# Kernel optimization log

Measured on AMD Instinct MI355X. Metric: run time of the kernel, lower is better.

Reference implementation:

```python
import jax, jax.numpy as jnp
import numpy as np

HIDDEN = 100  # hard-coded in the torch module


def setup_inputs() -> dict:
    key = jax.random.key(0)
    k1, k2, k3, k4, k5 = jax.random.split(key, 5)
    dims, N, M = 32, 4096, 8192
    centroids = jax.random.normal(k1, (N, dims), dtype=jnp.float32)
    x = jax.random.normal(k2, (M, dims), dtype=jnp.float32)
    # torch Linear params: y = x @ W.T (+ b)
    W1 = jax.random.normal(k3, (HIDDEN, dims), dtype=jnp.float32) / np.sqrt(dims)
    W2 = jax.random.normal(k4, (dims, HIDDEN), dtype=jnp.float32) / np.sqrt(HIDDEN)
    b2 = jax.random.uniform(k5, (dims,), dtype=jnp.float32, minval=-0.1, maxval=0.1)
    return {"centroids": centroids, "x": x, "W1": W1, "W2": W2, "b2": b2}


def reference(centroids, x, W1, W2, b2):
    dims = centroids.shape[1]
    # small MLP: Linear(dims,100,no bias) -> Linear(100,dims) -> tanh, then gate by centroids
    loc = jnp.tanh((centroids @ W1.T) @ W2.T + b2) * centroids  # [N, dims]
    # covariance = eye(dims) * var(centroids) (scalar, unbiased var over all elements)
    var = jnp.var(centroids, ddof=1)
    # diagonal-Gaussian log_prob, pairwise [N, M] via ||x-loc||^2 expansion (no NxMxD cube)
    sq = (
        jnp.sum(x * x, axis=1)[None, :]
        + jnp.sum(loc * loc, axis=1)[:, None]
        - 2.0 * (loc @ x.T)
    )  # [N, M]
    log_norm = dims * jnp.log(2.0 * jnp.pi * var)
    logp = -0.5 * (sq / var + log_norm)  # [N, M]
    return jnp.exp(logp).T  # [M, N]
```

## Files before the change

### kernel.cpp

```cpp
#include <hip/hip_runtime.h>
#include <math.h>

#define DIMS 32
#define NROWS 4096
#define MROWS 8192
#define HID 100

#define L2E 1.44269504088896340736f

typedef float f32x4 __attribute__((ext_vector_type(4)));
typedef short bf16x8 __attribute__((ext_vector_type(8)));

__device__ __forceinline__ void load_var(const float* part, float& iv, float& var) {
    float S = 0.0f, Q = 0.0f;
    #pragma unroll
    for (int i = 0; i < 8; i++) { S += part[2 * i]; Q += part[2 * i + 1]; }
    const float cnt = (float)(NROWS * DIMS);
    var = (Q - S * S / cnt) / (cnt - 1.0f);
    iv = 1.0f / var;
}

__device__ __forceinline__ float tanh_fast(float x) {
    float xc = fminf(fmaxf(x, -10.0f), 10.0f);
    float e = __builtin_amdgcn_exp2f(xc * (2.0f * L2E));
    return (e - 1.0f) * __builtin_amdgcn_rcpf(e + 1.0f);
}

__device__ __forceinline__ unsigned short f2bf(float f) {
    unsigned int u = __float_as_uint(f);
    u += 0x7FFFu + ((u >> 16) & 1u);
    return (unsigned short)(u >> 16);
}

__global__ __launch_bounds__(256) void k_prep(const float* __restrict__ cent,
                                              const float* __restrict__ x,
                                              const float* __restrict__ W1,
                                              const float* __restrict__ W2,
                                              const float* __restrict__ b2,
                                              float* __restrict__ part,
                                              float* __restrict__ A,
                                              float* __restrict__ B,
                                              unsigned short* __restrict__ xb,
                                              unsigned short* __restrict__ locb) {
    int b = blockIdx.x, t = threadIdx.x;

    if (b < 8) {
        const float4* c4 = (const float4*)cent;
        float s = 0.0f, q = 0.0f;
        #pragma unroll
        for (int i = 0; i < 16; i++) {
            float4 a = c4[b * 4096 + i * 256 + t];
            s += a.x + a.y + a.z + a.w;
            q += a.x * a.x + a.y * a.y + a.z * a.z + a.w * a.w;
        }
        #pragma unroll
        for (int off = 32; off > 0; off >>= 1) {
            s += __shfl_down(s, off);
            q += __shfl_down(q, off);
        }
        __shared__ float red[8];
        int lane = t & 63, wid = t >> 6;
        if (lane == 0) { red[wid] = s; red[4 + wid] = q; }
        __syncthreads();
        if (t == 0) {
            part[2 * b]     = red[0] + red[1] + red[2] + red[3];
            part[2 * b + 1] = red[4] + red[5] + red[6] + red[7];
        }
    } else if (b < 24) {
        __shared__ float w1s[HID * DIMS];
        __shared__ float w2s[DIMS * HID];
        __shared__ __align__(16) float ms[DIMS * DIMS];
        __shared__ float b2s[DIMS];
        for (int i = t; i < HID * DIMS; i += 256) { w1s[i] = W1[i]; w2s[i] = W2[i]; }
        if (t < DIMS) b2s[t] = b2[t];
        __syncthreads();
        #pragma unroll
        for (int o = 0; o < 4; o++) {
            int id = o * 256 + t;
            int r = id >> 5, cc = id & 31;
            float a = 0.0f;
            for (int j = 0; j < HID; j++) a += w2s[r * HID + j] * w1s[j * DIMS + cc];
            ms[id] = a;
        }
        __syncthreads();

        int n = (b - 8) * 256 + t;
        float c[DIMS];
        const float4* cr = (const float4*)(cent + (size_t)n * DIMS);
        #pragma unroll
        for (int i = 0; i < 8; i++) {
            float4 v = cr[i];
            c[4 * i] = v.x; c[4 * i + 1] = v.y; c[4 * i + 2] = v.z; c[4 * i + 3] = v.w;
        }
        float lr[DIMS];
        float lsq = 0.0f;
        #pragma unroll
        for (int d = 0; d < DIMS; d++) {
            const float4* mr = (const float4*)&ms[d * DIMS];
            float a0 = 0.f, a1 = 0.f, a2 = 0.f, a3 = 0.f;
            #pragma unroll
            for (int kk = 0; kk < 8; kk++) {
                float4 m = mr[kk];
                a0 += c[4 * kk] * m.x;
                a1 += c[4 * kk + 1] * m.y;
                a2 += c[4 * kk + 2] * m.z;
                a3 += c[4 * kk + 3] * m.w;
            }
            float v = tanh_fast((a0 + a1) + (a2 + a3) + b2s[d]) * c[d];
            lr[d] = v;
            lsq += v * v;
        }
        unsigned int w[16];
        #pragma unroll
        for (int d = 0; d < 16; d++)
            w[d] = (unsigned int)f2bf(lr[2 * d]) | ((unsigned int)f2bf(lr[2 * d + 1]) << 16);
        uint4* lo = (uint4*)(locb + (size_t)n * DIMS);
        lo[0] = make_uint4(w[0], w[1], w[2], w[3]);
        lo[1] = make_uint4(w[4], w[5], w[6], w[7]);
        lo[2] = make_uint4(w[8], w[9], w[10], w[11]);
        lo[3] = make_uint4(w[12], w[13], w[14], w[15]);
        B[n] = lsq;
    } else {
        int m = (b - 24) * 256 + t;
        const float4* xr = (const float4*)(x + (size_t)m * DIMS);
        float xsq = 0.0f;
        unsigned int w[16];
        #pragma unroll
        for (int i = 0; i < 8; i++) {
            float4 v = xr[i];
            xsq += v.x * v.x + v.y * v.y + v.z * v.z + v.w * v.w;
            w[2 * i]     = (unsigned int)f2bf(v.x) | ((unsigned int)f2bf(v.y) << 16);
            w[2 * i + 1] = (unsigned int)f2bf(v.z) | ((unsigned int)f2bf(v.w) << 16);
        }
        uint4* xo = (uint4*)(xb + (size_t)m * DIMS);
        xo[0] = make_uint4(w[0], w[1], w[2], w[3]);
        xo[1] = make_uint4(w[4], w[5], w[6], w[7]);
        xo[2] = make_uint4(w[8], w[9], w[10], w[11]);
        xo[3] = make_uint4(w[12], w[13], w[14], w[15]);
        A[m] = xsq;
    }
}

__global__ __launch_bounds__(256) void k_pair(const unsigned short* __restrict__ xb,
                                              const unsigned short* __restrict__ locb,
                                              const float* __restrict__ A,
                                              const float* __restrict__ B,
                                              const float* __restrict__ part,
                                              float* __restrict__ out) {
    float iv, var;
    load_var(part, iv, var);
    const float s  = L2E * iv;
    const float hv = -0.5f * L2E * iv;
    const float C0 = -16.0f * log2f(2.0f * (float)M_PI * var);

    int t = threadIdx.x;
    int lane = t & 63, wid = t >> 6;
    int bid = blockIdx.x;
    int tile = ((bid & 7) << 8) | (bid >> 3);
    int mt = tile >> 5, ntl = tile & 31;
    int m0 = mt * 128 + (wid >> 1) * 64;
    int n0 = ntl * 128 + (wid & 1) * 64;
    int r = lane & 15, g = lane >> 4;

    bf16x8 lf[4], xf[4];
    #pragma unroll
    for (int j = 0; j < 4; j++)
        lf[j] = *(const bf16x8*)(locb + (size_t)(n0 + 16 * j + r) * DIMS + 8 * g);
    #pragma unroll
    for (int i = 0; i < 4; i++)
        xf[i] = *(const bf16x8*)(xb + (size_t)(m0 + 16 * i + r) * DIMS + 8 * g);

    f32x4 zero = {0.0f, 0.0f, 0.0f, 0.0f};
    f32x4 acc[4][4];
    #pragma unroll
    for (int j = 0; j < 4; j++)
        #pragma unroll
        for (int i = 0; i < 4; i++)
            acc[j][i] = __builtin_amdgcn_mfma_f32_16x16x32_bf16(lf[j], xf[i], zero, 0, 0, 0);

    float em[4];
    #pragma unroll
    for (int i = 0; i < 4; i++)
        em[i] = fmaf(hv, A[m0 + 16 * i + r], C0);
    f32x4 en[4];
    #pragma unroll
    for (int j = 0; j < 4; j++) {
        float4 bv = *(const float4*)&B[n0 + 16 * j + 4 * g];
        en[j].x = hv * bv.x; en[j].y = hv * bv.y; en[j].z = hv * bv.z; en[j].w = hv * bv.w;
    }

    #pragma unroll
    for (int i = 0; i < 4; i++) {
        float* orow = out + (size_t)(m0 + 16 * i + r) * NROWS;
        float e = em[i];
        #pragma unroll
        for (int j = 0; j < 4; j++) {
            f32x4 v;
            v.x = __builtin_amdgcn_exp2f(fmaf(s, acc[j][i][0], e + en[j].x));
            v.y = __builtin_amdgcn_exp2f(fmaf(s, acc[j][i][1], e + en[j].y));
            v.z = __builtin_amdgcn_exp2f(fmaf(s, acc[j][i][2], e + en[j].z));
            v.w = __builtin_amdgcn_exp2f(fmaf(s, acc[j][i][3], e + en[j].w));
            *(f32x4*)(orow + n0 + 16 * j + 4 * g) = v;
        }
    }
}

extern "C" void kernel_launch(void* const* d_in, const int* in_sizes, int n_in,
                              void* d_out, int out_size, void* d_ws, size_t ws_size,
                              hipStream_t stream) {
    const float* cent = (const float*)d_in[0];
    const float* x    = (const float*)d_in[1];
    const float* W1   = (const float*)d_in[2];
    const float* W2   = (const float*)d_in[3];
    const float* b2   = (const float*)d_in[4];
    float* out = (float*)d_out;

    float* ws   = (float*)d_ws;
    float* part = ws;
    float* A    = ws + 64;
    float* B    = A + MROWS;
    unsigned short* xb   = (unsigned short*)(B + NROWS);
    unsigned short* locb = xb + (size_t)MROWS * DIMS;

    k_prep<<<56, 256, 0, stream>>>(cent, x, W1, W2, b2, part, A, B, xb, locb);
    k_pair<<<NROWS / 128 * (MROWS / 128), 256, 0, stream>>>(xb, locb, A, B, part, out);
}
```

Measured before the change: 159.5 us.

## Fuse loc MLP and bf16 packing into pairwise kernel via shared memory

The prep kernel no longer writes bf16 loc/x and the squared norms to global memory. It now only computes the variance partials and the 32x32 combined weight matrix. Each pairwise tile block recomputes the MLP for its 128 centroids and packs its 128 x rows to bf16 in padded LDS, then runs the MFMA and exp epilogue. This removes the large prep kernel and a global round trip, at the cost of redundant MLP and conversion work in every one of the 2048 tile blocks. The prep critical path also shrinks to 8 blocks, with block 0 handling the weight product.

```diff
diff --git a/kernel.cpp b/kernel.cpp
--- a/kernel.cpp
+++ b/kernel.cpp
@@ -8,6 +8,8 @@
 
 #define L2E 1.44269504088896340736f
 
+#define LROW 40
+
 typedef float f32x4 __attribute__((ext_vector_type(4)));
 typedef short bf16x8 __attribute__((ext_vector_type(8)));
 
@@ -32,47 +34,37 @@
     return (unsigned short)(u >> 16);
 }
 
-__global__ __launch_bounds__(256) void k_prep(const float* __restrict__ cent,
-                                              const float* __restrict__ x,
-                                              const float* __restrict__ W1,
-                                              const float* __restrict__ W2,
-                                              const float* __restrict__ b2,
-                                              float* __restrict__ part,
-                                              float* __restrict__ A,
-                                              float* __restrict__ B,
-                                              unsigned short* __restrict__ xb,
-                                              unsigned short* __restrict__ locb) {
+__global__ __launch_bounds__(256) void k_var(const float* __restrict__ c,
+                                             const float* __restrict__ W1,
+                                             const float* __restrict__ W2,
+                                             float* __restrict__ part,
+                                             float* __restrict__ Mmat) {
     int b = blockIdx.x, t = threadIdx.x;
-
-    if (b < 8) {
-        const float4* c4 = (const float4*)cent;
-        float s = 0.0f, q = 0.0f;
-        #pragma unroll
-        for (int i = 0; i < 16; i++) {
-            float4 a = c4[b * 4096 + i * 256 + t];
-            s += a.x + a.y + a.z + a.w;
-            q += a.x * a.x + a.y * a.y + a.z * a.z + a.w * a.w;
-        }
-        #pragma unroll
-        for (int off = 32; off > 0; off >>= 1) {
-            s += __shfl_down(s, off);
-            q += __shfl_down(q, off);
-        }
-        __shared__ float red[8];
-        int lane = t & 63, wid = t >> 6;
-        if (lane == 0) { red[wid] = s; red[4 + wid] = q; }
-        __syncthreads();
-        if (t == 0) {
-            part[2 * b]     = red[0] + red[1] + red[2] + red[3];
-            part[2 * b + 1] = red[4] + red[5] + red[6] + red[7];
-        }
-    } else if (b < 24) {
+    const float4* c4 = (const float4*)c;
+    float s = 0.0f, q = 0.0f;
+    #pragma unroll
+    for (int i = 0; i < 16; i++) {
+        float4 a = c4[b * 4096 + i * 256 + t];
+        s += a.x + a.y + a.z + a.w;
+        q += a.x * a.x + a.y * a.y + a.z * a.z + a.w * a.w;
+    }
+    #pragma unroll
+    for (int off = 32; off > 0; off >>= 1) {
+        s += __shfl_down(s, off);
+        q += __shfl_down(q, off);
+    }
+    __shared__ float red[8];
+    int lane = t & 63, wid = t >> 6;
+    if (lane == 0) { red[wid] = s; red[4 + wid] = q; }
+    __syncthreads();
+    if (t == 0) {
+        part[2 * b]     = red[0] + red[1] + red[2] + red[3];
+        part[2 * b + 1] = red[4] + red[5] + red[6] + red[7];
+    }
+    if (b == 0) {
         __shared__ float w1s[HID * DIMS];
         __shared__ float w2s[DIMS * HID];
-        __shared__ __align__(16) float ms[DIMS * DIMS];
-        __shared__ float b2s[DIMS];
         for (int i = t; i < HID * DIMS; i += 256) { w1s[i] = W1[i]; w2s[i] = W2[i]; }
-        if (t < DIMS) b2s[t] = b2[t];
         __syncthreads();
         #pragma unroll
         for (int o = 0; o < 4; o++) {
@@ -80,13 +72,46 @@
             int r = id >> 5, cc = id & 31;
             float a = 0.0f;
             for (int j = 0; j < HID; j++) a += w2s[r * HID + j] * w1s[j * DIMS + cc];
-            ms[id] = a;
-        }
-        __syncthreads();
-
-        int n = (b - 8) * 256 + t;
+            Mmat[id] = a;
+        }
+    }
+}
+
+__global__ __launch_bounds__(256) void k_fused(const float* __restrict__ cent,
+                                               const float* __restrict__ x,
+                                               const float* __restrict__ b2,
+                                               const float* __restrict__ part,
+                                               const float* __restrict__ Mmat,
+                                               float* __restrict__ out) {
+    __shared__ __align__(16) float ms[DIMS * DIMS];
+    __shared__ float b2s[DIMS];
+    __shared__ __align__(16) unsigned short ls[128 * LROW];
+    __shared__ __align__(16) unsigned short xs[128 * LROW];
+    __shared__ float As[128];
+    __shared__ float Bs[128];
+
+    float iv, var;
+    load_var(part, iv, var);
+    const float s  = L2E * iv;
+    const float hv = -0.5f * L2E * iv;
+    const float C0 = -16.0f * log2f(2.0f * (float)M_PI * var);
+
+    int t = threadIdx.x;
+    int lane = t & 63, wid = t >> 6;
+    int bid = blockIdx.x;
+    int tile = ((bid & 7) << 8) | (bid >> 3);
+    int mt = tile >> 5, ntl = tile & 31;
+    int mb = mt * 128, nb = ntl * 128;
+
+    #pragma unroll
+    for (int i = 0; i < 4; i++) ms[i * 256 + t] = Mmat[i * 256 + t];
+    if (t < DIMS) b2s[t] = b2[t];
+    __syncthreads();
+
+    if (t < 128) {
+        int row = t;
         float c[DIMS];
-        const float4* cr = (const float4*)(cent + (size_t)n * DIMS);
+        const float4* cr = (const float4*)(cent + (size_t)(nb + row) * DIMS);
         #pragma unroll
         for (int i = 0; i < 8; i++) {
             float4 v = cr[i];
@@ -110,65 +135,53 @@
             lr[d] = v;
             lsq += v * v;
         }
-        unsigned int w[16];
-        #pragma unroll
-        for (int d = 0; d < 16; d++)
-            w[d] = (unsigned int)f2bf(lr[2 * d]) | ((unsigned int)f2bf(lr[2 * d + 1]) << 16);
-        uint4* lo = (uint4*)(locb + (size_t)n * DIMS);
-        lo[0] = make_uint4(w[0], w[1], w[2], w[3]);
-        lo[1] = make_uint4(w[4], w[5], w[6], w[7]);
-        lo[2] = make_uint4(w[8], w[9], w[10], w[11]);
-        lo[3] = make_uint4(w[12], w[13], w[14], w[15]);
-        B[n] = lsq;
+        uint4* lq = (uint4*)&ls[row * LROW];
+        #pragma unroll
+        for (int q = 0; q < 4; q++) {
+            uint4 w;
+            w.x = (unsigned int)f2bf(lr[8 * q + 0]) | ((unsigned int)f2bf(lr[8 * q + 1]) << 16);
+            w.y = (unsigned int)f2bf(lr[8 * q + 2]) | ((unsigned int)f2bf(lr[8 * q + 3]) << 16);
+            w.z = (unsigned int)f2bf(lr[8 * q + 4]) | ((unsigned int)f2bf(lr[8 * q + 5]) << 16);
+            w.w = (unsigned int)f2bf(lr[8 * q + 6]) | ((unsigned int)f2bf(lr[8 * q + 7]) << 16);
+            lq[q] = w;
+        }
+        Bs[row] = hv * lsq;
     } else {
-        int m = (b - 24) * 256 + t;
-        const float4* xr = (const float4*)(x + (size_t)m * DIMS);
+        int row = t - 128;
+        const float4* xr = (const float4*)(x + (size_t)(mb + row) * DIMS);
+        float xv[DIMS];
         float xsq = 0.0f;
-        unsigned int w[16];
         #pragma unroll
         for (int i = 0; i < 8; i++) {
             float4 v = xr[i];
+            xv[4 * i] = v.x; xv[4 * i + 1] = v.y; xv[4 * i + 2] = v.z; xv[4 * i + 3] = v.w;
             xsq += v.x * v.x + v.y * v.y + v.z * v.z + v.w * v.w;
-            w[2 * i]     = (unsigned int)f2bf(v.x) | ((unsigned int)f2bf(v.y) << 16);
-            w[2 * i + 1] = (unsigned int)f2bf(v.z) | ((unsigned int)f2bf(v.w) << 16);
-        }
-        uint4* xo = (uint4*)(xb + (size_t)m * DIMS);
-        xo[0] = make_uint4(w[0], w[1], w[2], w[3]);
-        xo[1] = make_uint4(w[4], w[5], w[6], w[7]);
-        xo[2] = make_uint4(w[8], w[9], w[10], w[11]);
-        xo[3] = make_uint4(w[12], w[13], w[14], w[15]);
-        A[m] = xsq;
-    }
-}
-
-__global__ __launch_bounds__(256) void k_pair(const unsigned short* __restrict__ xb,
-                                              const unsigned short* __restrict__ locb,
-                                              const float* __restrict__ A,
-                                              const float* __restrict__ B,
-                                              const float* __restrict__ part,
-                                              float* __restrict__ out) {
-    float iv, var;
-    load_var(part, iv, var);
-    const float s  = L2E * iv;
-    const float hv = -0.5f * L2E * iv;
-    const float C0 = -16.0f * log2f(2.0f * (float)M_PI * var);
-
-    int t = threadIdx.x;
-    int lane = t & 63, wid = t >> 6;
-    int bid = blockIdx.x;
-    int tile = ((bid & 7) << 8) | (bid >> 3);
-    int mt = tile >> 5, ntl = tile & 31;
-    int m0 = mt * 128 + (wid >> 1) * 64;
-    int n0 = ntl * 128 + (wid & 1) * 64;
+        }
+        uint4* xq = (uint4*)&xs[row * LROW];
+        #pragma unroll
+        for (int q = 0; q < 4; q++) {
+            uint4 w;
+            w.x = (unsigned int)f2bf(xv[8 * q + 0]) | ((unsigned int)f2bf(xv[8 * q + 1]) << 16);
+            w.y = (unsigned int)f2bf(xv[8 * q + 2]) | ((unsigned int)f2bf(xv[8 * q + 3]) << 16);
+            w.z = (unsigned int)f2bf(xv[8 * q + 4]) | ((unsigned int)f2bf(xv[8 * q + 5]) << 16);
+            w.w = (unsigned int)f2bf(xv[8 * q + 6]) | ((unsigned int)f2bf(xv[8 * q + 7]) << 16);
+            xq[q] = w;
+        }
+        As[row] = fmaf(hv, xsq, C0);
+    }
+    __syncthreads();
+
+    int ml = (wid >> 1) * 64;
+    int nl = (wid & 1) * 64;
     int r = lane & 15, g = lane >> 4;
 
     bf16x8 lf[4], xf[4];
     #pragma unroll
     for (int j = 0; j < 4; j++)
-        lf[j] = *(const bf16x8*)(locb + (size_t)(n0 + 16 * j + r) * DIMS + 8 * g);
+        lf[j] = *(const bf16x8*)&ls[(nl + 16 * j + r) * LROW + 8 * g];
     #pragma unroll
     for (int i = 0; i < 4; i++)
-        xf[i] = *(const bf16x8*)(xb + (size_t)(m0 + 16 * i + r) * DIMS + 8 * g);
+        xf[i] = *(const bf16x8*)&xs[(ml + 16 * i + r) * LROW + 8 * g];
 
     f32x4 zero = {0.0f, 0.0f, 0.0f, 0.0f};
     f32x4 acc[4][4];
@@ -180,18 +193,17 @@
 
     float em[4];
     #pragma unroll
-    for (int i = 0; i < 4; i++)
-        em[i] = fmaf(hv, A[m0 + 16 * i + r], C0);
+    for (int i = 0; i < 4; i++) em[i] = As[ml + 16 * i + r];
     f32x4 en[4];
     #pragma unroll
     for (int j = 0; j < 4; j++) {
-        float4 bv = *(const float4*)&B[n0 + 16 * j + 4 * g];
-        en[j].x = hv * bv.x; en[j].y = hv * bv.y; en[j].z = hv * bv.z; en[j].w = hv * bv.w;
+        float4 bv = *(const float4*)&Bs[nl + 16 * j + 4 * g];
+        en[j].x = bv.x; en[j].y = bv.y; en[j].z = bv.z; en[j].w = bv.w;
     }
 
     #pragma unroll
     for (int i = 0; i < 4; i++) {
-        float* orow = out + (size_t)(m0 + 16 * i + r) * NROWS;
+        float* orow = out + (size_t)(mb + ml + 16 * i + r) * NROWS + nb + nl;
         float e = em[i];
         #pragma unroll
         for (int j = 0; j < 4; j++) {
@@ -200,7 +212,7 @@
             v.y = __builtin_amdgcn_exp2f(fmaf(s, acc[j][i][1], e + en[j].y));
             v.z = __builtin_amdgcn_exp2f(fmaf(s, acc[j][i][2], e + en[j].z));
             v.w = __builtin_amdgcn_exp2f(fmaf(s, acc[j][i][3], e + en[j].w));
-            *(f32x4*)(orow + n0 + 16 * j + 4 * g) = v;
+            *(f32x4*)(orow + 16 * j + 4 * g) = v;
         }
     }
 }
@@ -217,11 +229,8 @@
 
     float* ws   = (float*)d_ws;
     float* part = ws;
-    float* A    = ws + 64;
-    float* B    = A + MROWS;
-    unsigned short* xb   = (unsigned short*)(B + NROWS);
-    unsigned short* locb = xb + (size_t)MROWS * DIMS;
-
-    k_prep<<<56, 256, 0, stream>>>(cent, x, W1, W2, b2, part, A, B, xb, locb);
-    k_pair<<<NROWS / 128 * (MROWS / 128), 256, 0, stream>>>(xb, locb, A, B, part, out);
-}
+    float* Mmat = ws + 64;
+
+    k_var<<<8, 256, 0, stream>>>(cent, W1, W2, part, Mmat);
+    k_fused<<<NROWS / 128 * (MROWS / 128), 256, 0, stream>>>(cent, x, b2, part, Mmat, out);
+}
```

Measured after the change: 176.4 us. +10.6%, slower.
